# Kernel optimization log

Measured on AMD Instinct MI355X. Metric: run time of the kernel, lower is better.

The kernel has to match this reference:

```python
import jax, jax.numpy as jnp
import numpy as np

B, H, W = 16, 1024, 1024
EPS = 1e-7
FG_PROB = 0.1  # foreground pixel probability for synthetic gt


def setup_inputs() -> dict:
    key = jax.random.key(0)
    k1, k2 = jax.random.split(key)
    probs = jax.random.normal(k1, (B, 2, H, W), dtype=jnp.float32)
    gt = (jax.random.uniform(k2, (B, H, W)) < FG_PROB).astype(jnp.float32)
    gt_f_num = gt.sum(axis=(1, 2))  # per-sample foreground pixel count (float)
    return {"probs": probs, "gt": gt, "gt_f_num": gt_f_num, "img_h": H, "img_w": W}


def reference(probs, gt, gt_f_num, img_h, img_w):
    # foreground probability, clamped
    pc = jax.nn.softmax(probs, axis=1)[:, 1, :, :]
    pc = jnp.clip(pc, EPS, 1.0 - EPS)
    b = pc.shape[0]
    f_loss = -(gt * jnp.log(pc)).reshape(b, -1)          # [B, N]
    b_loss = -((1.0 - gt) * jnp.log(1.0 - pc)).reshape(b, -1)  # [B, N]
    n = b_loss.shape[1]

    # sort background loss descending per sample; top gt_f_num[i] entries are
    # "difficult" negatives, the rest are "simple" (equivalent to the torch
    # gather-into-zero-buffers since only sums/counts are taken afterwards)
    sorted_b = -jnp.sort(-b_loss, axis=1)                # descending, [B, N]
    k = gt_f_num.astype(jnp.int32)                       # int(gt_f_num[i])
    mask = jnp.arange(n, dtype=jnp.int32)[None, :] < k[:, None]  # [B, N]

    difficult_sum = jnp.sum(jnp.where(mask, sorted_b, 0.0), axis=1)
    simple_sum = jnp.sum(jnp.where(mask, 0.0, sorted_b), axis=1)
    difficult_num = jnp.sum(mask & (sorted_b != 0.0), axis=1).astype(jnp.float32)

    difficult_b_loss = difficult_sum / (difficult_num + 1e-16)
    simple_b_loss = simple_sum / (float(img_h * img_w) + 1e-16)
    f_loss_mean = f_loss.sum(axis=1) / (gt_f_num + 1e-16)

    return difficult_b_loss.mean() + f_loss_mean.mean() + simple_b_loss.mean()
```

## Files before the change

kernel.cpp:

```cpp
#include <hip/hip_runtime.h>
#include <math.h>

#define NB 16
#define NPIX 1048576
#define BINS 4096
#define CHUNKS 64
#define TPB_A 512
#define PIX_PER_BLOCK (NPIX / CHUNKS)
#define TPB_B 256
#define BLOSS_MAX 16.2f
#define B_CAP 15.9424f
#define F_CAP 16.1181f

__device__ __forceinline__ void fadd_lds(float* p, float v) {
    __hip_atomic_fetch_add(p, v, __ATOMIC_RELAXED, __HIP_MEMORY_SCOPE_WORKGROUP);
}
__device__ __forceinline__ void fadd_glb(float* p, float v) {
    __hip_atomic_fetch_add(p, v, __ATOMIC_RELAXED, __HIP_MEMORY_SCOPE_AGENT);
}

__global__ __launch_bounds__(TPB_A) void pass_a(
    const float* __restrict__ probs, const float* __restrict__ gt,
    unsigned* __restrict__ g_cnt, float* __restrict__ g_sum,
    float* __restrict__ f_sum)
{
    __shared__ unsigned s_cnt[BINS];
    __shared__ float s_sum[BINS];
    __shared__ float s_red[TPB_A / 64];

    const int tid = threadIdx.x;
    for (int j = tid; j < BINS; j += TPB_A) { s_cnt[j] = 0u; s_sum[j] = 0.f; }
    __syncthreads();

    const int blk = blockIdx.x;
    const int b = blk / CHUNKS;
    const int chunk = blk % CHUNKS;
    const float* p0 = probs + (size_t)b * 2 * NPIX;
    const float* p1 = p0 + NPIX;
    const float* gp = gt + (size_t)b * NPIX;
    const int base = chunk * PIX_PER_BLOCK;
    const float scale = (float)BINS / BLOSS_MAX;

    float f_acc = 0.f;
    const int iters = PIX_PER_BLOCK / (TPB_A * 4);
    for (int it = 0; it < iters; ++it) {
        const int i = base + ((it * TPB_A + tid) << 2);
        const float4 a0 = *(const float4*)(p0 + i);
        const float4 a1 = *(const float4*)(p1 + i);
        const float4 gg = *(const float4*)(gp + i);
        float dv[4] = {a1.x - a0.x, a1.y - a0.y, a1.z - a0.z, a1.w - a0.w};
        float gv[4] = {gg.x, gg.y, gg.z, gg.w};
        #pragma unroll
        for (int q = 0; q < 4; ++q) {
            const float d = dv[q];
            const float t = __logf(1.f + __expf(-fabsf(d)));
            if (gv[q] > 0.5f) {
                f_acc += fminf(fmaxf(-d, 0.f) + t, F_CAP);
            } else {
                const float bl = fminf(fmaxf(d, 0.f) + t, B_CAP);
                int bin = (int)(bl * scale);
                bin = bin < (BINS - 1) ? bin : (BINS - 1);
                atomicAdd(&s_cnt[bin], 1u);
                fadd_lds(&s_sum[bin], bl);
            }
        }
    }
    __syncthreads();

    for (int j = tid; j < BINS; j += TPB_A) {
        const unsigned c = s_cnt[j];
        if (c) {
            atomicAdd(&g_cnt[(size_t)b * BINS + j], c);
            fadd_glb(&g_sum[(size_t)b * BINS + j], s_sum[j]);
        }
    }

    #pragma unroll
    for (int o = 32; o > 0; o >>= 1) f_acc += __shfl_down(f_acc, o, 64);
    if ((tid & 63) == 0) s_red[tid >> 6] = f_acc;
    __syncthreads();
    if (tid == 0) {
        float s = 0.f;
        #pragma unroll
        for (int w = 0; w < TPB_A / 64; ++w) s += s_red[w];
        fadd_glb(&f_sum[b], s);
    }
}

__global__ __launch_bounds__(TPB_B) void pass_b(
    const unsigned* __restrict__ g_cnt, const float* __restrict__ g_sum,
    const float* __restrict__ f_sum, const float* __restrict__ gt_f_num,
    float* __restrict__ terms)
{
    __shared__ unsigned s_cnt[BINS];
    __shared__ float s_sum[BINS];
    __shared__ unsigned s_ccnt[TPB_B];
    __shared__ double s_csum[TPB_B];

    const int b = blockIdx.x;
    const int t = threadIdx.x;

    for (int j = 0; j < BINS / TPB_B; ++j) {
        const int bin = j * TPB_B + t;
        s_cnt[bin] = g_cnt[(size_t)b * BINS + bin];
        s_sum[bin] = g_sum[(size_t)b * BINS + bin];
    }
    __syncthreads();

    {
        unsigned c = 0; double s = 0.0;
        #pragma unroll
        for (int j = 0; j < BINS / TPB_B; ++j) {
            c += s_cnt[t * (BINS / TPB_B) + j];
            s += (double)s_sum[t * (BINS / TPB_B) + j];
        }
        s_ccnt[t] = c; s_csum[t] = s;
    }
    __syncthreads();

    if (t == 0) {
        const float fs = f_sum[b];
        const long long kk = (long long)gt_f_num[b];
        unsigned long long n_pos = 0; double S_total = 0.0;
        for (int c = 0; c < TPB_B; ++c) { n_pos += s_ccnt[c]; S_total += s_csum[c]; }

        double difficult_sum, difficult_num;
        if (kk <= 0) {
            difficult_sum = 0.0; difficult_num = 0.0;
        } else if ((unsigned long long)kk >= n_pos) {
            difficult_sum = S_total; difficult_num = (double)n_pos;
        } else {
            unsigned long long cum = 0; double Sa = 0.0;
            int cc = TPB_B - 1;
            for (; cc >= 0; --cc) {
                if (cum + s_ccnt[cc] >= (unsigned long long)kk) break;
                cum += s_ccnt[cc]; Sa += s_csum[cc];
            }
            int bstar = cc * (BINS / TPB_B);
            for (int j = (BINS / TPB_B) - 1; j >= 0; --j) {
                const int bin = cc * (BINS / TPB_B) + j;
                if (cum + s_cnt[bin] >= (unsigned long long)kk) { bstar = bin; break; }
                cum += s_cnt[bin]; Sa += (double)s_sum[bin];
            }
            const double jtake = (double)(kk - (long long)cum);
            const double avg = (s_cnt[bstar] > 0)
                ? ((double)s_sum[bstar] / (double)s_cnt[bstar]) : 0.0;
            difficult_sum = Sa + jtake * avg;
            difficult_num = (double)kk;
        }

        const double simple_sum = S_total - difficult_sum;
        const double gfn = (double)gt_f_num[b];
        const double term = difficult_sum / (difficult_num + 1e-16)
                          + (double)fs / (gfn + 1e-16)
                          + simple_sum / ((double)NPIX + 1e-16);
        terms[b] = (float)term;
    }
}

__global__ void pass_c(const float* __restrict__ terms, float* __restrict__ out)
{
    if (threadIdx.x == 0 && blockIdx.x == 0) {
        float s = 0.f;
        #pragma unroll
        for (int i = 0; i < NB; ++i) s += terms[i];
        out[0] = s / (float)NB;
    }
}

extern "C" void kernel_launch(void* const* d_in, const int* in_sizes, int n_in,
                              void* d_out, int out_size, void* d_ws, size_t ws_size,
                              hipStream_t stream) {
    const float* probs = (const float*)d_in[0];
    const float* gt    = (const float*)d_in[1];
    const float* gfn   = (const float*)d_in[2];
    char* ws = (char*)d_ws;

    const size_t hist_elems = (size_t)NB * BINS;
    unsigned* g_cnt  = (unsigned*)ws;
    float*    g_sum  = (float*)(ws + hist_elems * 4);
    float*    f_sum  = (float*)(ws + hist_elems * 8);
    float*    terms  = f_sum + NB;

    hipMemsetAsync(ws, 0, hist_elems * 8 + NB * sizeof(float), stream);

    hipLaunchKernelGGL(pass_a, dim3(NB * CHUNKS), dim3(TPB_A), 0, stream,
                       probs, gt, g_cnt, g_sum, f_sum);
    hipLaunchKernelGGL(pass_b, dim3(NB), dim3(TPB_B), 0, stream,
                       g_cnt, g_sum, f_sum, gfn, terms);
    hipLaunchKernelGGL(pass_c, dim3(1), dim3(64), 0, stream,
                       terms, (float*)d_out);
}
```

Before: 276.3 us.

## Drop per-bin sum histogram, use bin midpoints, prefetch loads, parallel suffix scan

Removes the per-bin float sum histogram and its LDS and global float atomics. The background total is now accumulated per thread, and each bin's loss is approximated by its midpoint when computing the top-k difficult sum. The main loop now handles 8 pixels per thread and software-prefetches the next iteration's loads. The serial scan in the second pass becomes a parallel suffix scan. The midpoint approximation adds a small numerical error, bounded by half a bin width per element.

```diff
diff --git a/kernel.cpp b/kernel.cpp
--- a/kernel.cpp
+++ b/kernel.cpp
@@ -7,29 +7,30 @@
 #define CHUNKS 64
 #define TPB_A 512
 #define PIX_PER_BLOCK (NPIX / CHUNKS)
+#define PPT 8
+#define ITERS_A (PIX_PER_BLOCK / (TPB_A * PPT))
 #define TPB_B 256
+#define BINS_PER_CHUNK (BINS / TPB_B)
 #define BLOSS_MAX 16.2f
+#define BINW (BLOSS_MAX / (float)BINS)
 #define B_CAP 15.9424f
 #define F_CAP 16.1181f
 
-__device__ __forceinline__ void fadd_lds(float* p, float v) {
-    __hip_atomic_fetch_add(p, v, __ATOMIC_RELAXED, __HIP_MEMORY_SCOPE_WORKGROUP);
-}
 __device__ __forceinline__ void fadd_glb(float* p, float v) {
     __hip_atomic_fetch_add(p, v, __ATOMIC_RELAXED, __HIP_MEMORY_SCOPE_AGENT);
 }
 
 __global__ __launch_bounds__(TPB_A) void pass_a(
     const float* __restrict__ probs, const float* __restrict__ gt,
-    unsigned* __restrict__ g_cnt, float* __restrict__ g_sum,
-    float* __restrict__ f_sum)
+    unsigned* __restrict__ g_cnt, float* __restrict__ f_sum,
+    float* __restrict__ b_sum)
 {
     __shared__ unsigned s_cnt[BINS];
-    __shared__ float s_sum[BINS];
-    __shared__ float s_red[TPB_A / 64];
+    __shared__ float s_redf[TPB_A / 64];
+    __shared__ float s_redb[TPB_A / 64];
 
     const int tid = threadIdx.x;
-    for (int j = tid; j < BINS; j += TPB_A) { s_cnt[j] = 0u; s_sum[j] = 0.f; }
+    for (int j = tid; j < BINS; j += TPB_A) s_cnt[j] = 0u;
     __syncthreads();
 
     const int blk = blockIdx.x;
@@ -41,119 +42,138 @@
     const int base = chunk * PIX_PER_BLOCK;
     const float scale = (float)BINS / BLOSS_MAX;
 
-    float f_acc = 0.f;
-    const int iters = PIX_PER_BLOCK / (TPB_A * 4);
-    for (int it = 0; it < iters; ++it) {
-        const int i = base + ((it * TPB_A + tid) << 2);
-        const float4 a0 = *(const float4*)(p0 + i);
-        const float4 a1 = *(const float4*)(p1 + i);
-        const float4 gg = *(const float4*)(gp + i);
-        float dv[4] = {a1.x - a0.x, a1.y - a0.y, a1.z - a0.z, a1.w - a0.w};
-        float gv[4] = {gg.x, gg.y, gg.z, gg.w};
+    float f_acc = 0.f, b_acc = 0.f;
+
+    float4 cA0, cB0, cA1, cB1, cG0, cG1;
+    {
+        const int i = base + (tid << 2);
+        const int i2 = i + TPB_A * 4;
+        cA0 = *(const float4*)(p0 + i);  cB0 = *(const float4*)(p0 + i2);
+        cA1 = *(const float4*)(p1 + i);  cB1 = *(const float4*)(p1 + i2);
+        cG0 = *(const float4*)(gp + i);  cG1 = *(const float4*)(gp + i2);
+    }
+    for (int it = 0; it < ITERS_A; ++it) {
+        float4 nA0, nB0, nA1, nB1, nG0, nG1;
+        {
+            const int nit = (it + 1 < ITERS_A) ? it + 1 : it;
+            const int i = base + nit * (TPB_A * PPT) + (tid << 2);
+            const int i2 = i + TPB_A * 4;
+            nA0 = *(const float4*)(p0 + i);  nB0 = *(const float4*)(p0 + i2);
+            nA1 = *(const float4*)(p1 + i);  nB1 = *(const float4*)(p1 + i2);
+            nG0 = *(const float4*)(gp + i);  nG1 = *(const float4*)(gp + i2);
+        }
+        const float dv[PPT] = {cA1.x - cA0.x, cA1.y - cA0.y, cA1.z - cA0.z, cA1.w - cA0.w,
+                               cB1.x - cB0.x, cB1.y - cB0.y, cB1.z - cB0.z, cB1.w - cB0.w};
+        const float gv[PPT] = {cG0.x, cG0.y, cG0.z, cG0.w, cG1.x, cG1.y, cG1.z, cG1.w};
         #pragma unroll
-        for (int q = 0; q < 4; ++q) {
+        for (int q = 0; q < PPT; ++q) {
             const float d = dv[q];
-            const float t = __logf(1.f + __expf(-fabsf(d)));
+            const float sp = fmaxf(d, 0.f) + __logf(1.f + __expf(-fabsf(d)));
             if (gv[q] > 0.5f) {
-                f_acc += fminf(fmaxf(-d, 0.f) + t, F_CAP);
+                f_acc += fminf(sp - d, F_CAP);
             } else {
-                const float bl = fminf(fmaxf(d, 0.f) + t, B_CAP);
+                const float bl = fminf(sp, B_CAP);
+                b_acc += bl;
                 int bin = (int)(bl * scale);
                 bin = bin < (BINS - 1) ? bin : (BINS - 1);
                 atomicAdd(&s_cnt[bin], 1u);
-                fadd_lds(&s_sum[bin], bl);
             }
         }
+        cA0 = nA0; cB0 = nB0; cA1 = nA1; cB1 = nB1; cG0 = nG0; cG1 = nG1;
     }
     __syncthreads();
 
     for (int j = tid; j < BINS; j += TPB_A) {
         const unsigned c = s_cnt[j];
-        if (c) {
-            atomicAdd(&g_cnt[(size_t)b * BINS + j], c);
-            fadd_glb(&g_sum[(size_t)b * BINS + j], s_sum[j]);
-        }
+        if (c) atomicAdd(&g_cnt[(size_t)b * BINS + j], c);
     }
 
     #pragma unroll
-    for (int o = 32; o > 0; o >>= 1) f_acc += __shfl_down(f_acc, o, 64);
-    if ((tid & 63) == 0) s_red[tid >> 6] = f_acc;
+    for (int o = 32; o > 0; o >>= 1) {
+        f_acc += __shfl_down(f_acc, o, 64);
+        b_acc += __shfl_down(b_acc, o, 64);
+    }
+    if ((tid & 63) == 0) { s_redf[tid >> 6] = f_acc; s_redb[tid >> 6] = b_acc; }
     __syncthreads();
     if (tid == 0) {
-        float s = 0.f;
+        float f = 0.f, bs = 0.f;
         #pragma unroll
-        for (int w = 0; w < TPB_A / 64; ++w) s += s_red[w];
-        fadd_glb(&f_sum[b], s);
+        for (int w = 0; w < TPB_A / 64; ++w) { f += s_redf[w]; bs += s_redb[w]; }
+        fadd_glb(&f_sum[b], f);
+        fadd_glb(&b_sum[b], bs);
     }
 }
 
 __global__ __launch_bounds__(TPB_B) void pass_b(
-    const unsigned* __restrict__ g_cnt, const float* __restrict__ g_sum,
-    const float* __restrict__ f_sum, const float* __restrict__ gt_f_num,
+    const unsigned* __restrict__ g_cnt, const float* __restrict__ f_sum,
+    const float* __restrict__ b_sum, const float* __restrict__ gt_f_num,
     float* __restrict__ terms)
 {
     __shared__ unsigned s_cnt[BINS];
-    __shared__ float s_sum[BINS];
-    __shared__ unsigned s_ccnt[TPB_B];
-    __shared__ double s_csum[TPB_B];
+    __shared__ unsigned s_suf[TPB_B];
+    __shared__ double s_wsuf[TPB_B];
+    __shared__ double s_dsum;
 
     const int b = blockIdx.x;
     const int t = threadIdx.x;
 
-    for (int j = 0; j < BINS / TPB_B; ++j) {
+    for (int j = 0; j < BINS_PER_CHUNK; ++j) {
         const int bin = j * TPB_B + t;
         s_cnt[bin] = g_cnt[(size_t)b * BINS + bin];
-        s_sum[bin] = g_sum[(size_t)b * BINS + bin];
-    }
-    __syncthreads();
-
-    {
-        unsigned c = 0; double s = 0.0;
-        #pragma unroll
-        for (int j = 0; j < BINS / TPB_B; ++j) {
-            c += s_cnt[t * (BINS / TPB_B) + j];
-            s += (double)s_sum[t * (BINS / TPB_B) + j];
+    }
+    __syncthreads();
+
+    unsigned c = 0; double w = 0.0;
+    const int cb = t * BINS_PER_CHUNK;
+    for (int j = 0; j < BINS_PER_CHUNK; ++j) {
+        const unsigned cc = s_cnt[cb + j];
+        c += cc;
+        w += (double)cc * (double)(((float)(cb + j) + 0.5f) * BINW);
+    }
+    s_suf[t] = c; s_wsuf[t] = w;
+    __syncthreads();
+
+    for (int off = 1; off < TPB_B; off <<= 1) {
+        const unsigned ac = (t + off < TPB_B) ? s_suf[t + off] : 0u;
+        const double aw = (t + off < TPB_B) ? s_wsuf[t + off] : 0.0;
+        __syncthreads();
+        s_suf[t] += ac; s_wsuf[t] += aw;
+        __syncthreads();
+    }
+
+    const long long kk = (long long)gt_f_num[b];
+    const unsigned long long n_pos = (unsigned long long)s_suf[0];
+    const unsigned long long suf_me = s_suf[t];
+    const unsigned long long suf_nx = (t + 1 < TPB_B) ? s_suf[t + 1] : 0ull;
+
+    if (kk > 0 && (unsigned long long)kk < n_pos &&
+        suf_nx < (unsigned long long)kk && (unsigned long long)kk <= suf_me) {
+        unsigned long long cum = suf_nx;
+        double W = (t + 1 < TPB_B) ? s_wsuf[t + 1] : 0.0;
+        int bstar = cb;
+        for (int j = BINS_PER_CHUNK - 1; j >= 0; --j) {
+            const int bin = cb + j;
+            const unsigned cc = s_cnt[bin];
+            if (cum + cc >= (unsigned long long)kk) { bstar = bin; break; }
+            cum += cc;
+            W += (double)cc * (double)(((float)bin + 0.5f) * BINW);
         }
-        s_ccnt[t] = c; s_csum[t] = s;
+        const double partial = (double)(kk - (long long)cum);
+        s_dsum = W + partial * (double)(((float)bstar + 0.5f) * BINW);
     }
     __syncthreads();
 
     if (t == 0) {
-        const float fs = f_sum[b];
-        const long long kk = (long long)gt_f_num[b];
-        unsigned long long n_pos = 0; double S_total = 0.0;
-        for (int c = 0; c < TPB_B; ++c) { n_pos += s_ccnt[c]; S_total += s_csum[c]; }
-
-        double difficult_sum, difficult_num;
-        if (kk <= 0) {
-            difficult_sum = 0.0; difficult_num = 0.0;
-        } else if ((unsigned long long)kk >= n_pos) {
-            difficult_sum = S_total; difficult_num = (double)n_pos;
-        } else {
-            unsigned long long cum = 0; double Sa = 0.0;
-            int cc = TPB_B - 1;
-            for (; cc >= 0; --cc) {
-                if (cum + s_ccnt[cc] >= (unsigned long long)kk) break;
-                cum += s_ccnt[cc]; Sa += s_csum[cc];
-            }
-            int bstar = cc * (BINS / TPB_B);
-            for (int j = (BINS / TPB_B) - 1; j >= 0; --j) {
-                const int bin = cc * (BINS / TPB_B) + j;
-                if (cum + s_cnt[bin] >= (unsigned long long)kk) { bstar = bin; break; }
-                cum += s_cnt[bin]; Sa += (double)s_sum[bin];
-            }
-            const double jtake = (double)(kk - (long long)cum);
-            const double avg = (s_cnt[bstar] > 0)
-                ? ((double)s_sum[bstar] / (double)s_cnt[bstar]) : 0.0;
-            difficult_sum = Sa + jtake * avg;
-            difficult_num = (double)kk;
-        }
-
-        const double simple_sum = S_total - difficult_sum;
+        const double S_total = (double)b_sum[b];
+        const double fs = (double)f_sum[b];
         const double gfn = (double)gt_f_num[b];
-        const double term = difficult_sum / (difficult_num + 1e-16)
-                          + (double)fs / (gfn + 1e-16)
-                          + simple_sum / ((double)NPIX + 1e-16);
+        double dsum, dnum;
+        if (kk <= 0) { dsum = 0.0; dnum = 0.0; }
+        else if ((unsigned long long)kk >= n_pos) { dsum = S_total; dnum = (double)n_pos; }
+        else { dsum = s_dsum; dnum = (double)kk; }
+        const double term = dsum / (dnum + 1e-16)
+                          + fs / (gfn + 1e-16)
+                          + (S_total - dsum) / ((double)NPIX + 1e-16);
         terms[b] = (float)term;
     }
 }
@@ -176,18 +196,18 @@
     const float* gfn   = (const float*)d_in[2];
     char* ws = (char*)d_ws;
 
-    const size_t hist_elems = (size_t)NB * BINS;
-    unsigned* g_cnt  = (unsigned*)ws;
-    float*    g_sum  = (float*)(ws + hist_elems * 4);
-    float*    f_sum  = (float*)(ws + hist_elems * 8);
-    float*    terms  = f_sum + NB;
-
-    hipMemsetAsync(ws, 0, hist_elems * 8 + NB * sizeof(float), stream);
+    const size_t hist_bytes = (size_t)NB * BINS * 4;
+    unsigned* g_cnt = (unsigned*)ws;
+    float*    f_sum = (float*)(ws + hist_bytes);
+    float*    b_sum = f_sum + NB;
+    float*    terms = b_sum + NB;
+
+    hipMemsetAsync(ws, 0, hist_bytes + 2 * NB * sizeof(float), stream);
 
     hipLaunchKernelGGL(pass_a, dim3(NB * CHUNKS), dim3(TPB_A), 0, stream,
-                       probs, gt, g_cnt, g_sum, f_sum);
+                       probs, gt, g_cnt, f_sum, b_sum);
     hipLaunchKernelGGL(pass_b, dim3(NB), dim3(TPB_B), 0, stream,
-                       g_cnt, g_sum, f_sum, gfn, terms);
+                       g_cnt, f_sum, b_sum, gfn, terms);
     hipLaunchKernelGGL(pass_c, dim3(1), dim3(64), 0, stream,
                        terms, (float*)d_out);
 }
```

After: 244.2 us. 1.13x faster.
